# Performance work log

Hardware: AMD Instinct MI355X
Metric: run time of the kernel (lower is better)

## Reference

```python
import jax, jax.numpy as jnp
import numpy as np

CG_ITERS = 10
CG_TOL = 1e-5
ZPF = 3

def _to_c(x):
    return jax.lax.complex(x[..., 0], x[..., 1])

def _ata(img, csm, mask_c, wpsf_c, lam):
    # img: [nr, nc, ns] complex; csm: [C, nr, nc, ns]; mask_c/wpsf_c: [nr*ZPF, nc, ns]
    nrow_pad = mask_c.shape[0]
    hz = (ZPF - 1) * nrow_pad // ZPF // 2          # = nrow_pad // 3 (zero-pad per side)
    nrow_img = nrow_pad // ZPF
    SF = np.float32(np.sqrt(nrow_pad * mask_c.shape[1] * mask_c.shape[2]))
    coil = csm * img[None]                          # [C, nr, nc, ns]
    zp = jnp.pad(coil, ((0, 0), (hz, hz), (0, 0), (0, 0)))
    ksp = jnp.fft.fftn(zp, axes=(-3, -2, -1)) / SF
    wav = jnp.fft.fftn(wpsf_c[None] * jnp.fft.ifftn(ksp, axes=(-2, -1)), axes=(-2, -1))
    temp = wav * mask_c[None]
    unwav = jnp.fft.fftn(jnp.conj(wpsf_c)[None] * jnp.fft.ifftn(temp, axes=(-2, -1)), axes=(-2, -1))
    coil_imgs = jnp.fft.ifftn(unwav, axes=(-3, -2, -1)) * SF
    crop = coil_imgs[:, hz:hz + nrow_img]           # middle third of padded rows
    comb = jnp.sum(crop * jnp.conj(csm), axis=0)
    return comb + lam * img

def _cg(rhs_c, csm, mask_c, wpsf_c, lam):
    def body(carry, _):
        x, r, p, rTr = carry
        Ap = _ata(p, csm, mask_c, wpsf_c, lam)
        alpha = rTr / jnp.sum(jnp.conj(p) * Ap).real
        x1 = x + alpha * p
        r1 = r - alpha * Ap
        rTr1 = jnp.sum(jnp.conj(r1) * r1).real
        beta = rTr1 / rTr
        p1 = r1 + beta * p
        act = rTr > CG_TOL
        carry = (jnp.where(act, x1, x), jnp.where(act, r1, r),
                 jnp.where(act, p1, p), jnp.where(act, rTr1, rTr))
        return carry, None
    x0 = jnp.zeros_like(rhs_c)
    rTr0 = jnp.sum(jnp.conj(rhs_c) * rhs_c).real
    (x, _, _, _), _ = jax.lax.scan(body, (x0, rhs_c, rhs_c, rTr0), None, length=CG_ITERS)
    return x

def setup_inputs() -> dict:
    key = jax.random.key(0)
    k1, k2, k3, k4 = jax.random.split(key, 4)
    B, C, NR, NC, NS = 2, 12, 96, 96, 48
    rhs = jax.random.normal(k1, (B, NR, NC, NS, 2), dtype=jnp.float32)
    csm = jax.random.normal(k2, (B, C, NR, NC, NS, 2), dtype=jnp.float32) * 0.3
    mask = (jax.random.uniform(k3, (B, ZPF * NR, NC, NS)) < 0.33).astype(jnp.float32)
    wPSF = jax.random.normal(k4, (B, ZPF * NR, NC, NS, 2), dtype=jnp.float32)
    lam1 = jnp.full((1,), 0.03, dtype=jnp.float32)
    return {"rhs": rhs, "csm": csm, "mask": mask, "wPSF": wPSF, "lam1": lam1}

def reference(rhs, csm, mask, wPSF, lam1):
    lam = lam1[0]
    rhs_c = _to_c(rhs)
    csm_c = _to_c(csm)
    wpsf_c = _to_c(wPSF)
    mask_c = jax.lax.complex(mask, jnp.zeros_like(mask))
    per = lambda r, c, m, w: _cg(r, c, m, w, lam)
    x = jax.vmap(per)(rhs_c, csm_c, mask_c, wpsf_c)   # [B, nr, nc, ns] complex
    return jnp.stack([x.real, x.imag], axis=-1)
```

## Files before the change

kernel.cpp:

```cpp
#include <hip/hip_runtime.h>
#include <hip/hip_fp16.h>

typedef float2 cplx;
typedef __half2 gpak;

constexpr int B_   = 2;
constexpr int C_   = 12;
constexpr int NR   = 96;
constexpr int NC_  = 96;
constexpr int NS   = 48;
constexpr int NP   = 288;
constexpr int NCOL = NC_ * NS;
constexpr int NVOX = NR * NCOL;
constexpr int HV   = NVOX / 2;
constexpr int TILE = 64;
constexpr int TILES = NCOL / TILE;
constexpr int LSTR = 49;
constexpr int NSL  = C_;
constexpr float PI2 = 6.28318530717958647692f;
constexpr float R96 = 1.f/96.f, R48 = 1.f/48.f, R288 = 1.f/288.f;

#define RTR(it) (8 + 2*(it))
#define PAP(it) (32 + 2*(it))
#define PN(it)  (52 + 2*(it))

__device__ inline cplx cmulc(cplx a, cplx b){ return make_float2(a.x*b.x - a.y*b.y, a.x*b.y + a.y*b.x); }
__device__ inline cplx cmuljc(cplx a, cplx b){ return make_float2(a.x*b.x + a.y*b.y, a.y*b.x - a.x*b.y); }
__device__ inline cplx caddc(cplx a, cplx b){ return make_float2(a.x+b.x, a.y+b.y); }
__device__ inline cplx csubc(cplx a, cplx b){ return make_float2(a.x-b.x, a.y-b.y); }

__device__ __forceinline__ gpak pack_g(cplx v){ return __float22half2_rn(v); }
__device__ __forceinline__ cplx unpack_g(gpak h){ return __half22float2(h); }

union hpair { float2 f; gpak h[2]; };

__device__ inline void atomAddF(float* p, float v){
    __hip_atomic_fetch_add(p, v, __ATOMIC_RELAXED, __HIP_MEMORY_SCOPE_AGENT);
}

__device__ __forceinline__ cplx twf(float k, float rN){
    float s, c; __sincosf(-PI2 * k * rN, &s, &c);
    return make_float2(c, s);
}

template<bool INV>
__device__ __forceinline__ cplx w16k(int k){
    constexpr float re[10] = {1.f, 0.92387953251f, 0.70710678119f, 0.38268343236f, 0.f,
                              -0.38268343236f, -0.70710678119f, -0.92387953251f, -1.f, -0.92387953251f};
    constexpr float im[10] = {0.f, -0.38268343236f, -0.70710678119f, -0.92387953251f, -1.f,
                              -0.92387953251f, -0.70710678119f, -0.38268343236f, 0.f, 0.38268343236f};
    return make_float2(re[k], INV ? -im[k] : im[k]);
}
template<bool INV>
__device__ __forceinline__ cplx w6k(int k){
    const float rr = (k == 1) ? 0.5f : -0.5f;
    const float ii = INV ? 0.86602540378f : -0.86602540378f;
    return make_float2(rr, ii);
}
template<bool INV>
__device__ __forceinline__ void r4(cplx& a0, cplx& a1, cplx& a2, cplx& a3){
    cplx t0 = caddc(a0, a2), t1 = csubc(a0, a2);
    cplx t2 = caddc(a1, a3), t3 = csubc(a1, a3);
    cplx it3 = INV ? make_float2(-t3.y, t3.x) : make_float2(t3.y, -t3.x);
    a0 = caddc(t0, t2); a1 = caddc(t1, it3);
    a2 = csubc(t0, t2); a3 = csubc(t1, it3);
}
template<bool INV>
__device__ __forceinline__ void r3(cplx& a0, cplx& a1, cplx& a2){
    cplx t1 = caddc(a1, a2), t2 = csubc(a1, a2);
    cplx m1 = make_float2(a0.x - 0.5f * t1.x, a0.y - 0.5f * t1.y);
    const float s3 = INV ? -0.8660254037844386f : 0.8660254037844386f;
    cplx b1 = make_float2(m1.x + s3 * t2.y, m1.y - s3 * t2.x);
    cplx b2 = make_float2(m1.x - s3 * t2.y, m1.y + s3 * t2.x);
    a0 = caddc(a0, t1); a1 = b1; a2 = b2;
}
template<bool INV>
__device__ __forceinline__ void dft16(cplx x[16]){
    cplx y[16];
    #pragma unroll
    for (int j = 0; j < 4; ++j){
        cplx a0 = x[j], a1 = x[j+4], a2 = x[j+8], a3 = x[j+12];
        r4<INV>(a0, a1, a2, a3);
        y[4*j+0] = a0;
        y[4*j+1] = (j == 0) ? a1 : cmulc(a1, w16k<INV>(j));
        y[4*j+2] = (j == 0) ? a2 : cmulc(a2, w16k<INV>(2*j));
        y[4*j+3] = (j == 0) ? a3 : cmulc(a3, w16k<INV>(3*j));
    }
    #pragma unroll
    for (int q = 0; q < 4; ++q){
        cplx a0 = y[q], a1 = y[q+4], a2 = y[q+8], a3 = y[q+12];
        r4<INV>(a0, a1, a2, a3);
        x[q] = a0; x[q+4] = a1; x[q+8] = a2; x[q+12] = a3;
    }
}
template<bool INV>
__device__ __forceinline__ void dft6(cplx x[6]){
    cplx y[6];
    { cplx a0 = x[0], a1 = x[2], a2 = x[4]; r3<INV>(a0, a1, a2); y[0] = a0; y[1] = a1; y[2] = a2; }
    { cplx a0 = x[1], a1 = x[3], a2 = x[5]; r3<INV>(a0, a1, a2);
      y[3] = a0; y[4] = cmulc(a1, w6k<INV>(1)); y[5] = cmulc(a2, w6k<INV>(2)); }
    #pragma unroll
    for (int q = 0; q < 3; ++q){
        cplx s = caddc(y[q], y[q+3]), d = csubc(y[q], y[q+3]);
        x[q] = s; x[q+3] = d;
    }
}

template<int NW>
__device__ inline float block_reduce(float v){
    #pragma unroll
    for (int o = 32; o >= 1; o >>= 1) v += __shfl_down(v, o, 64);
    __shared__ float sh[NW];
    const int lane = threadIdx.x & 63, wv = threadIdx.x >> 6;
    if (lane == 0) sh[wv] = v;
    __syncthreads();
    float s = 0.f;
    if (threadIdx.x == 0){
        #pragma unroll
        for (int w = 0; w < NW; ++w) s += sh[w];
    }
    return s;
}

__global__ __launch_bounds__(512, 4)
void k_fwd(const gpak* __restrict__ ph, const gpak* __restrict__ csh,
           gpak* __restrict__ g, int cg0, int ncg, int ncga)
{
    __shared__ cplx A[NR * TILE];
    __shared__ cplx t96[96];
    __shared__ cplx t288[288];
    const int tid = threadIdx.x, bid = blockIdx.x;
    if (tid < 96) t96[tid] = twf((float)tid, R96);
    if (tid < 288) t288[tid] = twf((float)tid, R288);

    const int tile = bid % TILES;
    const int rem = bid / TILES;
    const int gc = rem % ncg, b = rem / ncg, c = cg0 + gc;
    const int colbase = tile * TILE;
    const gpak* pp = ph  + (size_t)b * NVOX;
    const gpak* cs = csh + ((size_t)b * C_ + c) * NVOX;
    gpak* gg = g + (size_t)(b * ncga + gc) * ((size_t)NP * NCOL);

    cplx xr[2][6];
    #pragma unroll
    for (int it = 0; it < 2; ++it){
        const int id = tid + it * 512;
        const int m = id >> 6, col = id & 63;
        #pragma unroll
        for (int v = 0; v < 6; ++v){
            const int gi = (m + 16*v) * NCOL + colbase + col;
            xr[it][v] = cmulc(unpack_g(pp[gi]), unpack_g(cs[gi]));
        }
    }
    __syncthreads();

    for (int a = 0; a < 3; ++a){
        if (a) __syncthreads();
        #pragma unroll
        for (int it = 0; it < 2; ++it){
            const int id = tid + it * 512;
            const int m = id >> 6, col = id & 63;
            cplx xv[6];
            if (a){
                #pragma unroll
                for (int v = 0; v < 6; ++v)
                    xv[v] = cmulc(xr[it][v], t288[a * (m + 16*v)]);
            } else {
                #pragma unroll
                for (int v = 0; v < 6; ++v) xv[v] = xr[it][v];
            }
            dft6<false>(xv);
            cplx* dst = &A[m * TILE + col];
            dst[0] = xv[0];
            #pragma unroll
            for (int r = 1; r < 6; ++r)
                dst[16*r*TILE] = cmulc(xv[r], t96[m * r]);
        }
        __syncthreads();
        if (tid < 384){
            const int r = tid >> 6, col = tid & 63;
            cplx d[16];
            #pragma unroll
            for (int m = 0; m < 16; ++m) d[m] = A[(m + 16*r) * TILE + col];
            dft16<false>(d);
            const cplx pref = t96[32 * a];
            #pragma unroll
            for (int t = 0; t < 16; ++t)
                gg[(size_t)(18*t + 3*r + a) * NCOL + colbase + col] = pack_g(cmulc(d[t], pref));
        }
    }
}

__global__ __launch_bounds__(512, 4)
void k_plane(gpak* __restrict__ g, const gpak* __restrict__ wh,
             const __half* __restrict__ pmh, int ncg, int ncga)
{
    __shared__ cplx A[NC_ * LSTR];
    __shared__ cplx t96[96];
    __shared__ cplx t48[48];
    const int tid = threadIdx.x, bid = blockIdx.x;
    if (tid < 96) t96[tid] = twf((float)tid, R96);
    else if (tid >= 128 && tid < 176) t48[tid - 128] = twf((float)(tid - 128), R48);

    const int rp = bid % NP;
    const int rem = bid / NP;
    const int gc = rem % ncg, b = rem / ncg;
    gpak* gg = g + ((size_t)(b * ncga + gc) * NP + rp) * NCOL;
    const gpak*  wp  = wh  + ((size_t)b * NP + rp) * NCOL;
    const __half* pmv = pmh + ((size_t)b * NP + rp) * NCOL;
    __syncthreads();

    #pragma unroll
    for (int it = 0; it < 3; ++it){
        const int id = tid + it * 512;
        const int m = id & 15, nc = id >> 4;
        cplx xv[3];
        #pragma unroll
        for (int v = 0; v < 3; ++v){
            const int e = nc * NS + m + 16*v;
            xv[v] = cmulc(unpack_g(gg[e]), unpack_g(wp[e]));
        }
        r3<false>(xv[0], xv[1], xv[2]);
        cplx* dst = &A[nc * LSTR + m];
        dst[0]  = xv[0];
        dst[16] = cmulc(xv[1], t48[m]);
        dst[32] = cmulc(xv[2], t48[2*m]);
    }
    __syncthreads();
    if (tid < 288){
        const int rho = tid / 96, nc = tid - rho * 96;
        cplx* pA = &A[nc * LSTR + 16 * rho];
        cplx d[16];
        #pragma unroll
        for (int m = 0; m < 16; ++m) d[m] = pA[m];
        dft16<false>(d);
        #pragma unroll
        for (int t = 0; t < 16; ++t) pA[t] = d[t];
    }
    __syncthreads();
    #pragma unroll
    for (int it = 0; it < 2; ++it){
        const int id = tid + it * 512;
        if (id < 768){
            const int m = id / NS, ns = id - m * NS;
            cplx xv[6];
            #pragma unroll
            for (int v = 0; v < 6; ++v) xv[v] = A[(m + 16*v) * LSTR + ns];
            dft6<false>(xv);
            A[m * LSTR + ns] = xv[0];
            #pragma unroll
            for (int r = 1; r < 6; ++r)
                A[(m + 16*r) * LSTR + ns] = cmulc(xv[r], t96[m * r]);
        }
    }
    __syncthreads();
    if (tid < 288){
        const int r = tid / NS, ns = tid - r * NS;
        cplx d[16];
        #pragma unroll
        for (int m = 0; m < 16; ++m) d[m] = A[(m + 16*r) * LSTR + ns];
        dft16<false>(d);
        #pragma unroll
        for (int t = 0; t < 16; ++t){
            const float mval = __half2float(pmv[(6*t + r) * NS + ns]);
            d[t].x *= mval; d[t].y *= mval;
        }
        dft16<true>(d);
        #pragma unroll
        for (int m = 0; m < 16; ++m) A[(m + 16*r) * LSTR + ns] = d[m];
    }
    __syncthreads();
    #pragma unroll
    for (int it = 0; it < 2; ++it){
        const int id = tid + it * 512;
        if (id < 768){
            const int m = id / NS, ns = id - m * NS;
            cplx xv[6];
            xv[0] = A[m * LSTR + ns];
            #pragma unroll
            for (int r = 1; r < 6; ++r){
                cplx w = t96[m * r]; w.y = -w.y;
                xv[r] = cmulc(A[(m + 16*r) * LSTR + ns], w);
            }
            dft6<true>(xv);
            #pragma unroll
            for (int v = 0; v < 6; ++v) A[(m + 16*v) * LSTR + ns] = xv[v];
        }
    }
    __syncthreads();
    if (tid < 288){
        const int rho = tid / 96, nc = tid - rho * 96;
        cplx* pA = &A[nc * LSTR + 16 * rho];
        cplx d[16];
        #pragma unroll
        for (int t = 0; t < 16; ++t) d[t] = pA[t];
        dft16<true>(d);
        #pragma unroll
        for (int m = 0; m < 16; ++m) pA[m] = d[m];
    }
    __syncthreads();
    #pragma unroll
    for (int it = 0; it < 3; ++it){
        const int id = tid + it * 512;
        const int m = id & 15, nc = id >> 4;
        cplx w1 = t48[m];   w1.y = -w1.y;
        cplx w2 = t48[2*m]; w2.y = -w2.y;
        cplx xv[3];
        xv[0] = A[nc * LSTR + m];
        xv[1] = cmulc(A[nc * LSTR + m + 16], w1);
        xv[2] = cmulc(A[nc * LSTR + m + 32], w2);
        r3<true>(xv[0], xv[1], xv[2]);
        #pragma unroll
        for (int v = 0; v < 3; ++v){
            const int e = nc * NS + m + 16*v;
            gg[e] = pack_g(cmuljc(xv[v], unpack_g(wp[e])));
        }
    }
}

__global__ __launch_bounds__(512, 3)
void k_inv(const gpak* __restrict__ g, const gpak* __restrict__ csh,
           const gpak* __restrict__ ph, gpak* __restrict__ ap,
           float* __restrict__ sc, int cg0, int ncg, int ncga, int iter)
{
    __shared__ cplx A[NR * TILE];
    __shared__ cplx t96[96];
    __shared__ cplx t288[288];
    const int tid = threadIdx.x, bid = blockIdx.x;
    if (tid < 96) t96[tid] = twf((float)tid, R96);
    if (tid < 288) t288[tid] = twf((float)tid, R288);

    const int tile = bid % TILES;
    const int rem = bid / TILES;
    const int gc = rem % ncg, b = rem / ncg;
    const int c = cg0 + gc;
    const int slice = c;
    const int colbase = tile * TILE;

    const gpak* gc_ = g + (size_t)(b * ncga + gc) * ((size_t)NP * NCOL);
    const gpak* cs  = csh + ((size_t)b * C_ + c) * NVOX;

    cplx accT[2][6];
    #pragma unroll
    for (int it = 0; it < 2; ++it)
        #pragma unroll
        for (int j = 0; j < 6; ++j) accT[it][j] = make_float2(0.f, 0.f);
    __syncthreads();

    for (int a = 0; a < 3; ++a){
        if (a) __syncthreads();
        if (tid < 384){
            const int c6 = tid >> 6, col = tid & 63;
            cplx d[16];
            #pragma unroll
            for (int u = 0; u < 16; ++u)
                d[u] = unpack_g(gc_[(size_t)(3*(c6 + 6*u) + a) * NCOL + colbase + col]);
            dft16<true>(d);
            #pragma unroll
            for (int q = 0; q < 16; ++q) A[(c6 + 6*q) * TILE + col] = d[q];
        }
        __syncthreads();
        #pragma unroll
        for (int it = 0; it < 2; ++it){
            const int id = tid + it * 512;
            const int q = id >> 6, col = id & 63;
            cplx xv[6];
            xv[0] = A[(6*q) * TILE + col];
            #pragma unroll
            for (int cc = 1; cc < 6; ++cc){
                cplx w = t96[q * cc]; w.y = -w.y;
                xv[cc] = cmulc(A[(cc + 6*q) * TILE + col], w);
            }
            dft6<true>(xv);
            if (a == 0){
                #pragma unroll
                for (int j = 0; j < 6; ++j){
                    const int gi = (q + 16*j) * NCOL + colbase + col;
                    accT[it][j] = caddc(accT[it][j], cmuljc(xv[j], unpack_g(cs[gi])));
                }
            } else {
                int idx = a * (q + 96);
                const int stp = 16 * a;
                #pragma unroll
                for (int j = 0; j < 6; ++j){
                    const int gi = (q + 16*j) * NCOL + colbase + col;
                    cplx f = t288[idx]; f.y = -f.y;
                    accT[it][j] = caddc(accT[it][j], cmuljc(cmulc(xv[j], f), unpack_g(cs[gi])));
                    idx += stp; if (idx >= 288) idx -= 288;
                }
            }
        }
    }
    gpak* aps = ap + ((size_t)slice * B_ + b) * NVOX;
    const gpak* pb = ph + (size_t)b * NVOX;
    const float s288 = 1.f / 288.f;
    float dotloc = 0.f;
    #pragma unroll
    for (int it = 0; it < 2; ++it){
        const int id = tid + it * 512;
        const int q = id >> 6, col = id & 63;
        #pragma unroll
        for (int j = 0; j < 6; ++j){
            const int gi = (q + 16*j) * NCOL + colbase + col;
            cplx av = accT[it][j];
            av.x *= s288; av.y *= s288;
            aps[gi] = pack_g(av);
            const cplx pv = unpack_g(pb[gi]);
            dotloc += pv.x * av.x + pv.y * av.y;
        }
    }
    const float s = block_reduce<8>(dotloc);
    if (tid == 0) atomAddF(&sc[PAP(iter) + b], s);
}

__global__ __launch_bounds__(512)
void k_prep_csm(const cplx* __restrict__ csm, gpak* __restrict__ csh, int n)
{
    for (int i = blockIdx.x * 512 + threadIdx.x; i < n; i += gridDim.x * 512)
        csh[i] = pack_g(csm[i]);
}

__global__ __launch_bounds__(512)
void k_prep_wm(const cplx* __restrict__ wpsf, const float* __restrict__ mask,
               gpak* __restrict__ wh, __half* __restrict__ pmh)
{
    const int bid = blockIdx.x;
    const cplx*  wsrc = wpsf + (size_t)bid * NCOL;
    const float* mk   = mask + (size_t)bid * NCOL;
    gpak*   wdst = wh  + (size_t)bid * NCOL;
    __half* out  = pmh + (size_t)bid * NCOL;
    for (int e = threadIdx.x; e < NCOL; e += 512){
        wdst[e] = pack_g(wsrc[e]);
        const int knc = e / NS, pns = e - knc * NS;
        const int kns = 3 * (pns & 15) + (pns >> 4);
        out[e] = __float2half(mk[knc * NS + kns] * (1.f / 4608.f));
    }
}

__global__ __launch_bounds__(256)
void k_rr0(const cplx* __restrict__ rhs, cplx* __restrict__ r, cplx* __restrict__ p,
           gpak* __restrict__ ph, float* __restrict__ sc)
{
    const int i2 = blockIdx.x * 256 + threadIdx.x;
    const int b  = (int)(((size_t)blockIdx.x * 512) / NVOX);
    const float4 v4 = ((const float4*)rhs)[i2];
    ((float4*)r)[i2] = v4;
    ((float4*)p)[i2] = v4;
    hpair u;
    u.h[0] = pack_g(make_float2(v4.x, v4.y));
    u.h[1] = pack_g(make_float2(v4.z, v4.w));
    ((float2*)ph)[i2] = u.f;
    const float loc = v4.x*v4.x + v4.y*v4.y + v4.z*v4.z + v4.w*v4.w;
    const float s = block_reduce<4>(loc);
    if (threadIdx.x == 0){ atomAddF(&sc[RTR(0) + b], s); atomAddF(&sc[PN(0) + b], s); }
}

__global__ __launch_bounds__(256)
void k_update(cplx* __restrict__ x, cplx* __restrict__ r,
              const cplx* __restrict__ p, const gpak* __restrict__ ap,
              const float* __restrict__ lam1, float* __restrict__ sc, int it)
{
    const int i2 = blockIdx.x * 256 + threadIdx.x;
    const int b  = (int)(((size_t)blockIdx.x * 512) / NVOX);
    const int j2 = i2 - b * HV;
    const float rtr = sc[RTR(it) + b];
    const bool act = rtr > 1e-5f;
    const float lam = lam1[0];
    const float alpha = rtr / (sc[PAP(it) + b] + lam * sc[PN(it) + b]);

    const float4 pv4 = ((const float4*)p)[i2];
    cplx a0 = make_float2(lam * pv4.x, lam * pv4.y);
    cplx a1 = make_float2(lam * pv4.z, lam * pv4.w);
    #pragma unroll
    for (int gp = 0; gp < NSL; ++gp){
        hpair u;
        u.f = ((const float2*)(ap + ((size_t)gp * B_ + b) * NVOX))[j2];
        const cplx t0 = unpack_g(u.h[0]), t1 = unpack_g(u.h[1]);
        a0.x += t0.x; a0.y += t0.y;
        a1.x += t1.x; a1.y += t1.y;
    }
    float4 rv4 = ((const float4*)r)[i2];
    float loc = 0.f;
    if (act){
        float4 xv4 = ((const float4*)x)[i2];
        xv4.x += alpha * pv4.x; xv4.y += alpha * pv4.y;
        xv4.z += alpha * pv4.z; xv4.w += alpha * pv4.w;
        ((float4*)x)[i2] = xv4;
        rv4.x -= alpha * a0.x; rv4.y -= alpha * a0.y;
        rv4.z -= alpha * a1.x; rv4.w -= alpha * a1.y;
        ((float4*)r)[i2] = rv4;
    }
    loc = rv4.x*rv4.x + rv4.y*rv4.y + rv4.z*rv4.z + rv4.w*rv4.w;
    const float s = block_reduce<4>(loc);
    if (threadIdx.x == 0) atomAddF(&sc[RTR(it+1) + b], s);
}

__global__ __launch_bounds__(256)
void k_pupd(cplx* __restrict__ p, gpak* __restrict__ ph,
            const cplx* __restrict__ r, float* __restrict__ sc, int it)
{
    const int i2 = blockIdx.x * 256 + threadIdx.x;
    const int b  = (int)(((size_t)blockIdx.x * 512) / NVOX);
    const float rtr = sc[RTR(it) + b];
    const bool act = rtr > 1e-5f;
    const float4 pv4 = ((const float4*)p)[i2];
    float loc;
    if (act){
        const float be = sc[RTR(it+1) + b] / rtr;
        const float4 rv4 = ((const float4*)r)[i2];
        float4 pn4;
        pn4.x = rv4.x + be * pv4.x; pn4.y = rv4.y + be * pv4.y;
        pn4.z = rv4.z + be * pv4.z; pn4.w = rv4.w + be * pv4.w;
        ((float4*)p)[i2] = pn4;
        hpair u;
        u.h[0] = pack_g(make_float2(pn4.x, pn4.y));
        u.h[1] = pack_g(make_float2(pn4.z, pn4.w));
        ((float2*)ph)[i2] = u.f;
        loc = pn4.x*pn4.x + pn4.y*pn4.y + pn4.z*pn4.z + pn4.w*pn4.w;
    } else {
        loc = pv4.x*pv4.x + pv4.y*pv4.y + pv4.z*pv4.z + pv4.w*pv4.w;
    }
    const float s = block_reduce<4>(loc);
    if (threadIdx.x == 0) atomAddF(&sc[PN(it+1) + b], s);
}

extern "C" void kernel_launch(void* const* d_in, const int* in_sizes, int n_in,
                              void* d_out, int out_size, void* d_ws, size_t ws_size,
                              hipStream_t stream)
{
    const cplx*  rhs  = (const cplx*)d_in[0];
    const cplx*  csm  = (const cplx*)d_in[1];
    const float* mask = (const float*)d_in[2];
    const cplx*  wpsf = (const cplx*)d_in[3];
    const float* lam1 = (const float*)d_in[4];

    const size_t vb   = (size_t)B_ * NVOX * sizeof(cplx);
    const size_t hv   = (size_t)B_ * NVOX * sizeof(gpak);
    const size_t pmb  = (size_t)B_ * NP * NCOL * sizeof(__half);
    const size_t whb  = (size_t)B_ * NP * NCOL * sizeof(gpak);
    const size_t cshb = (size_t)B_ * C_ * NVOX * sizeof(gpak);
    const size_t percoil = (size_t)B_ * NP * NCOL * sizeof(gpak);

    char* ws = (char*)d_ws;
    float* sc = (float*)ws;
    size_t off = 512;
    cplx* r    = (cplx*)(ws + off); off += vb;
    cplx* p    = (cplx*)(ws + off); off += vb;
    gpak* ph   = (gpak*)(ws + off); off += hv;
    __half* pmh = (__half*)(ws + off); off += pmb;
    gpak* ap   = (gpak*)(ws + off); off += (size_t)NSL * hv;
    gpak* csh  = (gpak*)(ws + off); off += cshb;
    gpak* wh   = (gpak*)(ws + off); off += whb;
    gpak* g    = (gpak*)(ws + off);
    cplx* x    = (cplx*)d_out;

    int ncga = 1;
    if (ws_size > off){
        size_t fit = (ws_size - off) / percoil;
        ncga = fit > (size_t)C_ ? C_ : (int)fit;
        if (ncga < 1) ncga = 1;
    }

    hipMemsetAsync(d_out, 0, vb, stream);
    hipMemsetAsync(sc, 0, 512, stream);
    k_prep_csm<<<(B_ * C_ * NVOX) / 512, 512, 0, stream>>>(csm, csh, B_ * C_ * NVOX);
    k_prep_wm<<<B_ * NP, 512, 0, stream>>>(wpsf, mask, wh, pmh);
    k_rr0<<<(B_ * NVOX) / 512, 256, 0, stream>>>(rhs, r, p, ph, sc);

    for (int it = 0; it < 10; ++it){
        for (int cg0 = 0; cg0 < C_; cg0 += ncga){
            const int ncg = (C_ - cg0 < ncga) ? (C_ - cg0) : ncga;
            k_fwd  <<<TILES * ncg * B_, 512, 0, stream>>>(ph, csh, g, cg0, ncg, ncga);
            k_plane<<<NP    * ncg * B_, 512, 0, stream>>>(g, wh, pmh, ncg, ncga);
            k_inv  <<<TILES * ncg * B_, 512, 0, stream>>>(g, csh, ph, ap, sc, cg0, ncg, ncga, it);
        }
        k_update<<<(B_ * NVOX) / 512, 256, 0, stream>>>(x, r, p, ap, lam1, sc, it);
        k_pupd  <<<(B_ * NVOX) / 512, 256, 0, stream>>>(p, ph, r, sc, it);
    }
}
```

Measured before the change: 3.581 ms.

## Fuse CG direction update into forward FFT kernel and drop fp32 p buffer

Removes the separate p-update kernel: k_fwd now computes p = r + beta*p_old on the fly from half-precision r and p_old, and the first coil group writes the new p and accumulates its norm. p is kept only in fp16 with ping-pong buffers, and k_update writes a half copy of r. This saves one launch and the fp32 p read/write traffic per iteration. In exchange, every coil-group block recomputes the update, and the iterate now uses half-precision p, which may change accuracy.

```diff
diff --git a/kernel.cpp b/kernel.cpp
--- a/kernel.cpp
+++ b/kernel.cpp
@@ -123,8 +123,10 @@
 }
 
 __global__ __launch_bounds__(512, 4)
-void k_fwd(const gpak* __restrict__ ph, const gpak* __restrict__ csh,
-           gpak* __restrict__ g, int cg0, int ncg, int ncga)
+void k_fwd(const gpak* __restrict__ rh, const gpak* __restrict__ pold,
+           gpak* __restrict__ pnew, const gpak* __restrict__ csh,
+           gpak* __restrict__ g, float* __restrict__ sc,
+           int cg0, int ncg, int ncga, int iter)
 {
     __shared__ cplx A[NR * TILE];
     __shared__ cplx t96[96];
@@ -137,10 +139,21 @@
     const int rem = bid / TILES;
     const int gc = rem % ncg, b = rem / ncg, c = cg0 + gc;
     const int colbase = tile * TILE;
-    const gpak* pp = ph  + (size_t)b * NVOX;
+    const gpak* rr = rh   + (size_t)b * NVOX;
+    const gpak* po = pold + (size_t)b * NVOX;
+    gpak*       pn = pnew + (size_t)b * NVOX;
     const gpak* cs = csh + ((size_t)b * C_ + c) * NVOX;
     gpak* gg = g + (size_t)(b * ncga + gc) * ((size_t)NP * NCOL);
 
+    float beta = 0.f;
+    bool act = true;
+    if (iter > 0){
+        const float ro = sc[RTR(iter-1) + b];
+        act  = ro > 1e-5f;
+        beta = sc[RTR(iter) + b] / ro;
+    }
+
+    float pnloc = 0.f;
     cplx xr[2][6];
     #pragma unroll
     for (int it = 0; it < 2; ++it){
@@ -149,7 +162,23 @@
         #pragma unroll
         for (int v = 0; v < 6; ++v){
             const int gi = (m + 16*v) * NCOL + colbase + col;
-            xr[it][v] = cmulc(unpack_g(pp[gi]), unpack_g(cs[gi]));
+            cplx pv;
+            if (iter > 0){
+                const cplx pd = unpack_g(po[gi]);
+                if (act){
+                    const cplx rv = unpack_g(rr[gi]);
+                    const gpak ph16 = pack_g(make_float2(rv.x + beta*pd.x, rv.y + beta*pd.y));
+                    pv = unpack_g(ph16);
+                    if (gc == 0) pn[gi] = ph16;
+                } else {
+                    pv = pd;
+                    if (gc == 0) pn[gi] = po[gi];
+                }
+                if (gc == 0) pnloc += pv.x*pv.x + pv.y*pv.y;
+            } else {
+                pv = unpack_g(po[gi]);
+            }
+            xr[it][v] = cmulc(pv, unpack_g(cs[gi]));
         }
     }
     __syncthreads();
@@ -189,6 +218,12 @@
                 gg[(size_t)(18*t + 3*r + a) * NCOL + colbase + col] = pack_g(cmulc(d[t], pref));
         }
     }
+
+    if (gc == 0 && iter > 0){
+        __syncthreads();
+        const float s = block_reduce<8>(pnloc);
+        if (tid == 0) atomAddF(&sc[PN(iter) + b], s);
+    }
 }
 
 __global__ __launch_bounds__(512, 4)
@@ -320,7 +355,7 @@
 
 __global__ __launch_bounds__(512, 3)
 void k_inv(const gpak* __restrict__ g, const gpak* __restrict__ csh,
-           const gpak* __restrict__ ph, gpak* __restrict__ ap,
+           const gpak* __restrict__ pcur, gpak* __restrict__ ap,
            float* __restrict__ sc, int cg0, int ncg, int ncga, int iter)
 {
     __shared__ cplx A[NR * TILE];
@@ -392,7 +427,7 @@
         }
     }
     gpak* aps = ap + ((size_t)slice * B_ + b) * NVOX;
-    const gpak* pb = ph + (size_t)b * NVOX;
+    const gpak* pb = pcur + (size_t)b * NVOX;
     const float s288 = 1.f / 288.f;
     float dotloc = 0.f;
     #pragma unroll
@@ -438,26 +473,31 @@
 }
 
 __global__ __launch_bounds__(256)
-void k_rr0(const cplx* __restrict__ rhs, cplx* __restrict__ r, cplx* __restrict__ p,
-           gpak* __restrict__ ph, float* __restrict__ sc)
+void k_rr0(const cplx* __restrict__ rhs, cplx* __restrict__ r, gpak* __restrict__ rh,
+           gpak* __restrict__ pha, float* __restrict__ sc)
 {
     const int i2 = blockIdx.x * 256 + threadIdx.x;
     const int b  = (int)(((size_t)blockIdx.x * 512) / NVOX);
     const float4 v4 = ((const float4*)rhs)[i2];
     ((float4*)r)[i2] = v4;
-    ((float4*)p)[i2] = v4;
     hpair u;
     u.h[0] = pack_g(make_float2(v4.x, v4.y));
     u.h[1] = pack_g(make_float2(v4.z, v4.w));
-    ((float2*)ph)[i2] = u.f;
-    const float loc = v4.x*v4.x + v4.y*v4.y + v4.z*v4.z + v4.w*v4.w;
-    const float s = block_reduce<4>(loc);
-    if (threadIdx.x == 0){ atomAddF(&sc[RTR(0) + b], s); atomAddF(&sc[PN(0) + b], s); }
+    ((float2*)rh)[i2] = u.f;
+    ((float2*)pha)[i2] = u.f;
+    const cplx q0 = unpack_g(u.h[0]), q1 = unpack_g(u.h[1]);
+    const float lrr = v4.x*v4.x + v4.y*v4.y + v4.z*v4.z + v4.w*v4.w;
+    const float lpn = q0.x*q0.x + q0.y*q0.y + q1.x*q1.x + q1.y*q1.y;
+    const float s1 = block_reduce<4>(lrr);
+    if (threadIdx.x == 0) atomAddF(&sc[RTR(0) + b], s1);
+    __syncthreads();
+    const float s2 = block_reduce<4>(lpn);
+    if (threadIdx.x == 0) atomAddF(&sc[PN(0) + b], s2);
 }
 
 __global__ __launch_bounds__(256)
-void k_update(cplx* __restrict__ x, cplx* __restrict__ r,
-              const cplx* __restrict__ p, const gpak* __restrict__ ap,
+void k_update(cplx* __restrict__ x, cplx* __restrict__ r, gpak* __restrict__ rh,
+              const gpak* __restrict__ pcur, const gpak* __restrict__ ap,
               const float* __restrict__ lam1, float* __restrict__ sc, int it)
 {
     const int i2 = blockIdx.x * 256 + threadIdx.x;
@@ -468,9 +508,11 @@
     const float lam = lam1[0];
     const float alpha = rtr / (sc[PAP(it) + b] + lam * sc[PN(it) + b]);
 
-    const float4 pv4 = ((const float4*)p)[i2];
-    cplx a0 = make_float2(lam * pv4.x, lam * pv4.y);
-    cplx a1 = make_float2(lam * pv4.z, lam * pv4.w);
+    hpair up;
+    up.f = ((const float2*)(pcur + (size_t)b * NVOX))[j2];
+    const cplx p0 = unpack_g(up.h[0]), p1 = unpack_g(up.h[1]);
+    cplx a0 = make_float2(lam * p0.x, lam * p0.y);
+    cplx a1 = make_float2(lam * p1.x, lam * p1.y);
     #pragma unroll
     for (int gp = 0; gp < NSL; ++gp){
         hpair u;
@@ -480,48 +522,22 @@
         a1.x += t1.x; a1.y += t1.y;
     }
     float4 rv4 = ((const float4*)r)[i2];
-    float loc = 0.f;
     if (act){
         float4 xv4 = ((const float4*)x)[i2];
-        xv4.x += alpha * pv4.x; xv4.y += alpha * pv4.y;
-        xv4.z += alpha * pv4.z; xv4.w += alpha * pv4.w;
+        xv4.x += alpha * p0.x; xv4.y += alpha * p0.y;
+        xv4.z += alpha * p1.x; xv4.w += alpha * p1.y;
         ((float4*)x)[i2] = xv4;
         rv4.x -= alpha * a0.x; rv4.y -= alpha * a0.y;
         rv4.z -= alpha * a1.x; rv4.w -= alpha * a1.y;
         ((float4*)r)[i2] = rv4;
     }
-    loc = rv4.x*rv4.x + rv4.y*rv4.y + rv4.z*rv4.z + rv4.w*rv4.w;
+    hpair w;
+    w.h[0] = pack_g(make_float2(rv4.x, rv4.y));
+    w.h[1] = pack_g(make_float2(rv4.z, rv4.w));
+    ((float2*)(rh + (size_t)b * NVOX))[j2] = w.f;
+    const float loc = rv4.x*rv4.x + rv4.y*rv4.y + rv4.z*rv4.z + rv4.w*rv4.w;
     const float s = block_reduce<4>(loc);
     if (threadIdx.x == 0) atomAddF(&sc[RTR(it+1) + b], s);
-}
-
-__global__ __launch_bounds__(256)
-void k_pupd(cplx* __restrict__ p, gpak* __restrict__ ph,
-            const cplx* __restrict__ r, float* __restrict__ sc, int it)
-{
-    const int i2 = blockIdx.x * 256 + threadIdx.x;
-    const int b  = (int)(((size_t)blockIdx.x * 512) / NVOX);
-    const float rtr = sc[RTR(it) + b];
-    const bool act = rtr > 1e-5f;
-    const float4 pv4 = ((const float4*)p)[i2];
-    float loc;
-    if (act){
-        const float be = sc[RTR(it+1) + b] / rtr;
-        const float4 rv4 = ((const float4*)r)[i2];
-        float4 pn4;
-        pn4.x = rv4.x + be * pv4.x; pn4.y = rv4.y + be * pv4.y;
-        pn4.z = rv4.z + be * pv4.z; pn4.w = rv4.w + be * pv4.w;
-        ((float4*)p)[i2] = pn4;
-        hpair u;
-        u.h[0] = pack_g(make_float2(pn4.x, pn4.y));
-        u.h[1] = pack_g(make_float2(pn4.z, pn4.w));
-        ((float2*)ph)[i2] = u.f;
-        loc = pn4.x*pn4.x + pn4.y*pn4.y + pn4.z*pn4.z + pn4.w*pn4.w;
-    } else {
-        loc = pv4.x*pv4.x + pv4.y*pv4.y + pv4.z*pv4.z + pv4.w*pv4.w;
-    }
-    const float s = block_reduce<4>(loc);
-    if (threadIdx.x == 0) atomAddF(&sc[PN(it+1) + b], s);
 }
 
 extern "C" void kernel_launch(void* const* d_in, const int* in_sizes, int n_in,
@@ -545,8 +561,9 @@
     float* sc = (float*)ws;
     size_t off = 512;
     cplx* r    = (cplx*)(ws + off); off += vb;
-    cplx* p    = (cplx*)(ws + off); off += vb;
-    gpak* ph   = (gpak*)(ws + off); off += hv;
+    gpak* rh   = (gpak*)(ws + off); off += hv;
+    gpak* pha  = (gpak*)(ws + off); off += hv;
+    gpak* phb  = (gpak*)(ws + off); off += hv;
     __half* pmh = (__half*)(ws + off); off += pmb;
     gpak* ap   = (gpak*)(ws + off); off += (size_t)NSL * hv;
     gpak* csh  = (gpak*)(ws + off); off += cshb;
@@ -565,16 +582,17 @@
     hipMemsetAsync(sc, 0, 512, stream);
     k_prep_csm<<<(B_ * C_ * NVOX) / 512, 512, 0, stream>>>(csm, csh, B_ * C_ * NVOX);
     k_prep_wm<<<B_ * NP, 512, 0, stream>>>(wpsf, mask, wh, pmh);
-    k_rr0<<<(B_ * NVOX) / 512, 256, 0, stream>>>(rhs, r, p, ph, sc);
+    k_rr0<<<(B_ * NVOX) / 512, 256, 0, stream>>>(rhs, r, rh, pha, sc);
 
     for (int it = 0; it < 10; ++it){
+        gpak* pold = (it == 0) ? pha : ((it & 1) ? pha : phb);
+        gpak* pcur = (it & 1) ? phb : pha;
         for (int cg0 = 0; cg0 < C_; cg0 += ncga){
             const int ncg = (C_ - cg0 < ncga) ? (C_ - cg0) : ncga;
-            k_fwd  <<<TILES * ncg * B_, 512, 0, stream>>>(ph, csh, g, cg0, ncg, ncga);
+            k_fwd  <<<TILES * ncg * B_, 512, 0, stream>>>(rh, pold, pcur, csh, g, sc, cg0, ncg, ncga, it);
             k_plane<<<NP    * ncg * B_, 512, 0, stream>>>(g, wh, pmh, ncg, ncga);
-            k_inv  <<<TILES * ncg * B_, 512, 0, stream>>>(g, csh, ph, ap, sc, cg0, ncg, ncga, it);
-        }
-        k_update<<<(B_ * NVOX) / 512, 256, 0, stream>>>(x, r, p, ap, lam1, sc, it);
-        k_pupd  <<<(B_ * NVOX) / 512, 256, 0, stream>>>(p, ph, r, sc, it);
-    }
-}
+            k_inv  <<<TILES * ncg * B_, 512, 0, stream>>>(g, csh, pcur, ap, sc, cg0, ncg, ncga, it);
+        }
+        k_update<<<(B_ * NVOX) / 512, 256, 0, stream>>>(x, r, rh, pcur, ap, lam1, sc, it);
+    }
+}
```

New measurement: 3.584 ms. No clear change (+0.1%).
